# Kernel optimization log

Measured on AMD Instinct MI355X. Metric: run time of the kernel, lower is better.

## Reference

```python
import jax, jax.numpy as jnp
import numpy as np

B, T, C = 2, 2048, 1024
H = 16
D = C // H  # head_dim = 64
SCALE = D ** -0.5


def setup_inputs() -> dict:
    key = jax.random.key(0)
    ks = jax.random.split(key, 5)
    x = jax.random.normal(ks[0], (B, T, C), dtype=jnp.float32)
    # causal mask: -inf above diagonal, 0 elsewhere (module checks mask == -inf)
    neg_inf = jnp.float32(-jnp.inf)
    causal = jnp.where(jnp.tril(jnp.ones((T, T), dtype=bool)), 0.0, neg_inf)
    mask = causal[None, None, :, :].astype(jnp.float32)  # [1,1,T,T]
    # xavier_normal for [C, C] linear weights: std = sqrt(2/(C+C))
    std = float(np.sqrt(2.0 / (C + C)))
    wq = jax.random.normal(ks[1], (C, C), dtype=jnp.float32) * std
    wk = jax.random.normal(ks[2], (C, C), dtype=jnp.float32) * std
    wv = jax.random.normal(ks[3], (C, C), dtype=jnp.float32) * std
    wo = jax.random.normal(ks[4], (C, C), dtype=jnp.float32) * std
    return {"x": x, "mask": mask, "wq": wq, "wk": wk, "wv": wv, "wo": wo}


def reference(x, mask, wq, wk, wv, wo):
    # torch nn.Linear: y = x @ W.T
    q = jnp.einsum('btc,oc->bto', x, wq).reshape(B, T, H, D).transpose(0, 2, 1, 3)
    k = jnp.einsum('btc,oc->bto', x, wk).reshape(B, T, H, D).transpose(0, 2, 1, 3)
    v = jnp.einsum('btc,oc->bto', x, wv).reshape(B, T, H, D).transpose(0, 2, 1, 3)
    scores = jnp.einsum('bhqd,bhkd->bhqk', q, k) * SCALE  # [B,H,T,T]
    scores = jnp.where(mask == -jnp.inf, -jnp.inf, scores)
    attn = jax.nn.softmax(scores, axis=-1)
    out = jnp.einsum('bhqk,bhkd->bhqd', attn, v)  # [B,H,T,D]
    out = out.transpose(0, 2, 1, 3).reshape(B, T, C)
    return jnp.einsum('btc,oc->bto', out, wo)
```

## Files before the change

### kernel.cpp

```cpp
#include <hip/hip_runtime.h>
#include <hip/hip_bf16.h>


typedef __bf16 bf16_t;
typedef __bf16 bf16x8 __attribute__((ext_vector_type(8)));
typedef __bf16 bf16x4 __attribute__((ext_vector_type(4)));
typedef __bf16 bf16x2 __attribute__((ext_vector_type(2)));
typedef float  f32x4  __attribute__((ext_vector_type(4)));
typedef unsigned u32x4 __attribute__((ext_vector_type(4)));

__device__ __forceinline__ void gload_lds16(const bf16_t* g, bf16_t* l) {
  __builtin_amdgcn_global_load_lds((__attribute__((address_space(1))) void*)g,
                                   (__attribute__((address_space(3))) void*)l, 16, 0, 0);
}

__device__ __forceinline__ unsigned pack_bf16(float a, float b) {
  bf16x2 v; v[0] = (bf16_t)a; v[1] = (bf16_t)b;
  return __builtin_bit_cast(unsigned, v);
}

__device__ __forceinline__ float fexp2(float x) { return __builtin_amdgcn_exp2f(x); }

__global__ __launch_bounds__(256) void cvt_all(
    const float* __restrict__ x,  const float* __restrict__ i0, const float* __restrict__ i1,
    const float* __restrict__ i2, const float* __restrict__ i3,
    bf16_t* __restrict__ ox, bf16_t* __restrict__ o0, bf16_t* __restrict__ o1,
    bf16_t* __restrict__ o2, bf16_t* __restrict__ o3) {
  int blk = blockIdx.x;
  const float* in; bf16_t* out; int i;
  if (blk < 4096) { in = x; out = ox; i = blk * 256 + threadIdx.x; }
  else {
    int wb = blk - 4096;
    int which = wb >> 10;
    in  = (which == 0) ? i0 : (which == 1) ? i1 : (which == 2) ? i2 : i3;
    out = (which == 0) ? o0 : (which == 1) ? o1 : (which == 2) ? o2 : o3;
    i = (wb & 1023) * 256 + threadIdx.x;
  }
  float4 v = reinterpret_cast<const float4*>(in)[i];
  bf16x4 o;
  o[0] = (bf16_t)v.x; o[1] = (bf16_t)v.y; o[2] = (bf16_t)v.z; o[3] = (bf16_t)v.w;
  reinterpret_cast<bf16x4*>(out)[i] = o;
}

__global__ __launch_bounds__(256) void gemm_bt(
    const bf16_t* __restrict__ A,
    const bf16_t* __restrict__ W0, const bf16_t* __restrict__ W1, const bf16_t* __restrict__ W2,
    bf16_t* __restrict__ O0, bf16_t* __restrict__ O1, bf16_t* __restrict__ O2)
{
  __shared__ alignas(16) bf16_t As[64 * 64];
  __shared__ alignas(16) bf16_t Bs[128 * 64];
  const int K = 1024;
  const int t = threadIdx.x;
  const int lane = t & 63;
  const int w = t >> 6;
  const int wr = w >> 1, wc = w & 1;
  const int lo = lane & 15, hi = lane >> 4;
  const int m0 = blockIdx.x * 64, n0 = blockIdx.y * 128;

  const int mode = blockIdx.z;
  const bf16_t* Bw = (mode == 0) ? W0 : (mode == 1) ? W1 : W2;
  bf16_t* outb     = (mode == 0) ? O0 : (mode == 1) ? O1 : O2;

  f32x4 acc[2][4] = {};
  const int srow = t >> 3;
  const int sch  = t & 7;

  for (int k0 = 0; k0 < K; k0 += 64) {
#pragma unroll
    for (int r = 0; r < 2; ++r) {
      int row = r * 32 + srow;
      gload_lds16(A + (size_t)(m0 + row) * K + k0 + sch * 8, &As[row * 64 + sch * 8]);
    }
#pragma unroll
    for (int r = 0; r < 4; ++r) {
      int row = r * 32 + srow;
      gload_lds16(Bw + (size_t)(n0 + row) * K + k0 + sch * 8, &Bs[row * 64 + sch * 8]);
    }
    __syncthreads();
#pragma unroll
    for (int ks = 0; ks < 2; ++ks) {
      bf16x8 af[2], bfr[4];
#pragma unroll
      for (int i = 0; i < 2; ++i)
        af[i] = *reinterpret_cast<const bf16x8*>(&As[(wr * 32 + i * 16 + lo) * 64 + ks * 32 + hi * 8]);
#pragma unroll
      for (int j = 0; j < 4; ++j)
        bfr[j] = *reinterpret_cast<const bf16x8*>(&Bs[(wc * 64 + j * 16 + lo) * 64 + ks * 32 + hi * 8]);
#pragma unroll
      for (int i = 0; i < 2; ++i)
#pragma unroll
        for (int j = 0; j < 4; ++j)
          acc[i][j] = __builtin_amdgcn_mfma_f32_16x16x32_bf16(af[i], bfr[j], acc[i][j], 0, 0, 0);
    }
    __syncthreads();
  }

  if (mode == 2) {
#pragma unroll
    for (int i = 0; i < 2; ++i)
#pragma unroll
      for (int j = 0; j < 4; ++j) {
        int m = m0 + wr * 32 + i * 16 + hi * 4;
        int n = n0 + wc * 64 + j * 16 + lo;
        int b = m >> 11, tq = m & 2047;
        int h = (n >> 6) & 15, d = n & 63;
        bf16x4 pk;
#pragma unroll
        for (int r = 0; r < 4; ++r) pk[r] = (bf16_t)acc[i][j][r];
        *reinterpret_cast<bf16x4*>(
            &outb[((size_t)(b * 16 + h) * 64 + d) * 2048 + tq]) = pk;
      }
  } else {
#pragma unroll
    for (int i = 0; i < 2; ++i)
#pragma unroll
      for (int j = 0; j < 4; ++j)
#pragma unroll
        for (int r = 0; r < 4; ++r) {
          int m = m0 + wr * 32 + i * 16 + hi * 4 + r;
          int n = n0 + wc * 64 + j * 16 + lo;
          float v = acc[i][j][r];
          int b = m >> 11, tq = m & 2047;
          int h = n >> 6,  d  = n & 63;
          if (mode == 0) v *= 0.18033688011f;
          outb[((size_t)(b * 16 + h) * 2048 + tq) * 64 + d] = (bf16_t)v;
        }
  }
}

__global__ __launch_bounds__(256) void gemm_out(
    const bf16_t* __restrict__ A, const bf16_t* __restrict__ Wt, float* __restrict__ OF)
{
  __shared__ alignas(16) bf16_t As[64 * 64];
  __shared__ alignas(16) bf16_t Bs[128 * 64];
  const int K = 1024;
  const int t = threadIdx.x;
  const int lane = t & 63;
  const int w = t >> 6;
  const int wr = w >> 1, wc = w & 1;
  const int lo = lane & 15, hi = lane >> 4;
  const int m0 = blockIdx.x * 64, n0 = blockIdx.y * 128;

  f32x4 acc[2][4] = {};
  const int srow = t >> 3;
  const int sch  = t & 7;

  for (int k0 = 0; k0 < K; k0 += 64) {
#pragma unroll
    for (int r = 0; r < 2; ++r) {
      int row = r * 32 + srow;
      gload_lds16(A + (size_t)(m0 + row) * K + k0 + sch * 8, &As[row * 64 + sch * 8]);
    }
#pragma unroll
    for (int r = 0; r < 4; ++r) {
      int row = r * 32 + srow;
      gload_lds16(Wt + (size_t)(n0 + row) * K + k0 + sch * 8, &Bs[row * 64 + sch * 8]);
    }
    __syncthreads();
#pragma unroll
    for (int ks = 0; ks < 2; ++ks) {
      bf16x8 af[2], bfr[4];
#pragma unroll
      for (int i = 0; i < 2; ++i)
        af[i] = *reinterpret_cast<const bf16x8*>(&As[(wr * 32 + i * 16 + lo) * 64 + ks * 32 + hi * 8]);
#pragma unroll
      for (int j = 0; j < 4; ++j)
        bfr[j] = *reinterpret_cast<const bf16x8*>(&Bs[(wc * 64 + j * 16 + lo) * 64 + ks * 32 + hi * 8]);
#pragma unroll
      for (int i = 0; i < 2; ++i)
#pragma unroll
        for (int j = 0; j < 4; ++j)
          acc[i][j] = __builtin_amdgcn_mfma_f32_16x16x32_bf16(af[i], bfr[j], acc[i][j], 0, 0, 0);
    }
    __syncthreads();
  }

#pragma unroll
  for (int i = 0; i < 2; ++i)
#pragma unroll
    for (int j = 0; j < 4; ++j)
#pragma unroll
      for (int r = 0; r < 4; ++r) {
        int m = m0 + wr * 32 + i * 16 + hi * 4 + r;
        int n = n0 + wc * 64 + j * 16 + lo;
        OF[(size_t)m * 1024 + n] = acc[i][j][r];
      }
}

#define SLAB 8832

__global__ __launch_bounds__(256) void attn_fwd(
    const bf16_t* __restrict__ Q,
    const bf16_t* __restrict__ Km,
    const bf16_t* __restrict__ Vt,
    bf16_t* __restrict__ att)
{
  __shared__ alignas(16) char smem[4 * SLAB];
  const int t = threadIdx.x, lane = t & 63, w = t >> 6;
  const int lo = lane & 15, h = lane >> 4;
  const int blk = blockIdx.x;
  const int item = (blk & 7) * 128 + (blk >> 3);
  const int bh = item >> 5;
  const int pr = item & 31;
  const bf16_t* Qb = Q  + (size_t)bh * 2048 * 64;
  const bf16_t* Kb = Km + (size_t)bh * 2048 * 64;
  const bf16_t* Vb = Vt + (size_t)bh * 64 * 2048;
  float* accW = (float*)(smem + w * SLAB);
  float* lW   = (float*)(smem + w * SLAB + 8704);
  const int b = bh >> 4, hd = bh & 15;
  const int prow = 8 * (lo >> 2) + (lo & 3);

  auto run_tile = [&](int q0) {
    bf16x8 qf[2][2];
#pragma unroll
    for (int qt = 0; qt < 2; ++qt)
#pragma unroll
      for (int ks = 0; ks < 2; ++ks)
        qf[qt][ks] = *reinterpret_cast<const bf16x8*>(
            &Qb[(size_t)(q0 + qt * 16 + lo) * 64 + ks * 32 + h * 8]);

    f32x4 acc[2][4] = {};
    float lp[2] = {};
    const int kend = q0 + 32;
    for (int kb = w * 64; kb < kend; kb += 256) {
      bf16x8 kf[2][4];
#pragma unroll
      for (int ks = 0; ks < 2; ++ks)
#pragma unroll
        for (int kt = 0; kt < 4; ++kt) {
          int krow = kb + 32 * (kt & 1) + 4 * (kt >> 1) + prow;
          kf[ks][kt] = *reinterpret_cast<const bf16x8*>(
              &Kb[(size_t)krow * 64 + ks * 32 + h * 8]);
        }
      bf16x8 vf[2][4];
#pragma unroll
      for (int kh = 0; kh < 2; ++kh)
#pragma unroll
        for (int dt = 0; dt < 4; ++dt)
          vf[kh][dt] = *reinterpret_cast<const bf16x8*>(
              &Vb[(size_t)(dt * 16 + lo) * 2048 + kb + kh * 32 + h * 8]);
      f32x4 s_t[4][2] = {};
#pragma unroll
      for (int ks = 0; ks < 2; ++ks)
#pragma unroll
        for (int kt = 0; kt < 4; ++kt)
#pragma unroll
          for (int qt = 0; qt < 2; ++qt)
            s_t[kt][qt] = __builtin_amdgcn_mfma_f32_16x16x32_bf16(kf[ks][kt], qf[qt][ks], s_t[kt][qt], 0, 0, 0);
      if (kb + 63 >= q0) {
#pragma unroll
        for (int kt = 0; kt < 4; ++kt)
#pragma unroll
          for (int qt = 0; qt < 2; ++qt)
#pragma unroll
            for (int r = 0; r < 4; ++r) {
              int kg = kb + 32 * (kt & 1) + 8 * h + 4 * (kt >> 1) + r;
              int qg = q0 + qt * 16 + lo;
              if (kg > qg) s_t[kt][qt][r] = -__builtin_inff();
            }
      }
#pragma unroll
      for (int kt = 0; kt < 4; ++kt)
#pragma unroll
        for (int qt = 0; qt < 2; ++qt)
#pragma unroll
          for (int r = 0; r < 4; ++r) {
            float p = fexp2(s_t[kt][qt][r]);
            s_t[kt][qt][r] = p;
            lp[qt] += p;
          }
#pragma unroll
      for (int ks2 = 0; ks2 < 2; ++ks2)
#pragma unroll
        for (int qt = 0; qt < 2; ++qt) {
          u32x4 au;
          au[0] = pack_bf16(s_t[ks2][qt][0], s_t[ks2][qt][1]);
          au[1] = pack_bf16(s_t[ks2][qt][2], s_t[ks2][qt][3]);
          au[2] = pack_bf16(s_t[ks2 + 2][qt][0], s_t[ks2 + 2][qt][1]);
          au[3] = pack_bf16(s_t[ks2 + 2][qt][2], s_t[ks2 + 2][qt][3]);
          bf16x8 pa = __builtin_bit_cast(bf16x8, au);
#pragma unroll
          for (int dt = 0; dt < 4; ++dt)
            acc[qt][dt] = __builtin_amdgcn_mfma_f32_16x16x32_bf16(pa, vf[ks2][dt], acc[qt][dt], 0, 0, 0);
        }
    }

    float lrow[2];
#pragma unroll
    for (int qt = 0; qt < 2; ++qt) {
      float v = lp[qt];
      v += __shfl_xor(v, 16);
      v += __shfl_xor(v, 32);
      lrow[qt] = v;
    }

#pragma unroll
    for (int qt = 0; qt < 2; ++qt) {
#pragma unroll
      for (int r = 0; r < 4; ++r) {
        int row = qt * 16 + h * 4 + r;
#pragma unroll
        for (int dt = 0; dt < 4; ++dt)
          accW[row * 68 + dt * 16 + lo] = acc[qt][dt][r];
      }
      if (h == 0) lW[qt * 16 + lo] = lrow[qt];
    }
    __syncthreads();

    {
      const int row = t >> 3, c0 = (t & 7) * 8;
      float lsum = 0.f, o[8] = {};
#pragma unroll
      for (int w2 = 0; w2 < 4; ++w2) {
        lsum += ((const float*)(smem + w2 * SLAB + 8704))[row];
        const float* a2 = (const float*)(smem + w2 * SLAB) + row * 68 + c0;
#pragma unroll
        for (int j = 0; j < 8; ++j) o[j] += a2[j];
      }
      float inv = 1.f / lsum;
      bf16x8 ov;
#pragma unroll
      for (int j = 0; j < 8; ++j) ov[j] = (bf16_t)(o[j] * inv);
      *reinterpret_cast<bf16x8*>(&att[((size_t)(b * 2048 + q0 + row)) * 1024 + hd * 64 + c0]) = ov;
    }
    __syncthreads();
  };

  run_tile((63 - pr) * 32);
  run_tile(pr * 32);
}

extern "C" void kernel_launch(void* const* d_in, const int* in_sizes, int n_in,
                              void* d_out, int out_size, void* d_ws, size_t ws_size,
                              hipStream_t stream) {
  (void)in_sizes; (void)n_in; (void)out_size; (void)ws_size;
  const float* x  = (const float*)d_in[0];
  const float* wq = (const float*)d_in[2];
  const float* wk = (const float*)d_in[3];
  const float* wv = (const float*)d_in[4];
  const float* wo = (const float*)d_in[5];
  float* out = (float*)d_out;

  char* ws = (char*)d_ws;
  const size_t SZ_X = (size_t)4096 * 1024 * 2;
  const size_t SZ_W = (size_t)1024 * 1024 * 2;
  bf16_t* xb  = (bf16_t*)(ws);
  bf16_t* wqb = (bf16_t*)(ws + SZ_X);
  bf16_t* wkb = (bf16_t*)(ws + SZ_X + 1 * SZ_W);
  bf16_t* wvb = (bf16_t*)(ws + SZ_X + 2 * SZ_W);
  bf16_t* wob = (bf16_t*)(ws + SZ_X + 3 * SZ_W);
  bf16_t* qw  = (bf16_t*)(ws + 1 * SZ_X + 4 * SZ_W);
  bf16_t* kw  = (bf16_t*)(ws + 2 * SZ_X + 4 * SZ_W);
  bf16_t* vtw = (bf16_t*)(ws + 3 * SZ_X + 4 * SZ_W);
  bf16_t* att = xb;

  cvt_all<<<8192, 256, 0, stream>>>(x, wq, wk, wv, wo, xb, wqb, wkb, wvb, wob);

  gemm_bt<<<dim3(64, 8, 3), 256, 0, stream>>>(xb, wqb, wkb, wvb, qw, kw, vtw);
  attn_fwd<<<1024, 256, 0, stream>>>(qw, kw, vtw, att);
  gemm_out<<<dim3(64, 8), 256, 0, stream>>>(att, wob, out);
}
```

Measured before the change: 146.0 us.

## Stage partial attention outputs in bf16 LDS and load K/V per sub-step

The per-wave partial output accumulators are now staged in shared memory as bf16 instead of fp32, roughly halving the LDS slab per wave, and the cross-wave reduction reads them with 16-byte vector loads. K and V fragments are loaded per k-slice just before use rather than all up front, which lowers live vector registers. Together these aim to cut LDS footprint and register pressure to raise occupancy. The cost is an extra bf16 rounding of the unnormalized partial sums before the reduction, and less load latency hiding because the loads are issued later.

```diff
diff --git a/kernel.cpp b/kernel.cpp
--- a/kernel.cpp
+++ b/kernel.cpp
@@ -187,7 +187,7 @@
       }
 }
 
-#define SLAB 8832
+#define SLAB 4736
 
 __global__ __launch_bounds__(256) void attn_fwd(
     const bf16_t* __restrict__ Q,
@@ -205,8 +205,8 @@
   const bf16_t* Qb = Q  + (size_t)bh * 2048 * 64;
   const bf16_t* Kb = Km + (size_t)bh * 2048 * 64;
   const bf16_t* Vb = Vt + (size_t)bh * 64 * 2048;
-  float* accW = (float*)(smem + w * SLAB);
-  float* lW   = (float*)(smem + w * SLAB + 8704);
+  bf16_t* accW = (bf16_t*)(smem + w * SLAB);
+  float*  lW   = (float*)(smem + w * SLAB + 4608);
   const int b = bh >> 4, hd = bh & 15;
   const int prow = 8 * (lo >> 2) + (lo & 3);
 
@@ -223,30 +223,22 @@
     float lp[2] = {};
     const int kend = q0 + 32;
     for (int kb = w * 64; kb < kend; kb += 256) {
-      bf16x8 kf[2][4];
-#pragma unroll
-      for (int ks = 0; ks < 2; ++ks)
+      f32x4 s_t[4][2] = {};
+#pragma unroll
+      for (int ks = 0; ks < 2; ++ks) {
+        bf16x8 kf[4];
 #pragma unroll
         for (int kt = 0; kt < 4; ++kt) {
           int krow = kb + 32 * (kt & 1) + 4 * (kt >> 1) + prow;
-          kf[ks][kt] = *reinterpret_cast<const bf16x8*>(
+          kf[kt] = *reinterpret_cast<const bf16x8*>(
               &Kb[(size_t)krow * 64 + ks * 32 + h * 8]);
         }
-      bf16x8 vf[2][4];
-#pragma unroll
-      for (int kh = 0; kh < 2; ++kh)
-#pragma unroll
-        for (int dt = 0; dt < 4; ++dt)
-          vf[kh][dt] = *reinterpret_cast<const bf16x8*>(
-              &Vb[(size_t)(dt * 16 + lo) * 2048 + kb + kh * 32 + h * 8]);
-      f32x4 s_t[4][2] = {};
-#pragma unroll
-      for (int ks = 0; ks < 2; ++ks)
 #pragma unroll
         for (int kt = 0; kt < 4; ++kt)
 #pragma unroll
           for (int qt = 0; qt < 2; ++qt)
-            s_t[kt][qt] = __builtin_amdgcn_mfma_f32_16x16x32_bf16(kf[ks][kt], qf[qt][ks], s_t[kt][qt], 0, 0, 0);
+            s_t[kt][qt] = __builtin_amdgcn_mfma_f32_16x16x32_bf16(kf[kt], qf[qt][ks], s_t[kt][qt], 0, 0, 0);
+      }
       if (kb + 63 >= q0) {
 #pragma unroll
         for (int kt = 0; kt < 4; ++kt)
@@ -270,7 +262,12 @@
             lp[qt] += p;
           }
 #pragma unroll
-      for (int ks2 = 0; ks2 < 2; ++ks2)
+      for (int ks2 = 0; ks2 < 2; ++ks2) {
+        bf16x8 vf[4];
+#pragma unroll
+        for (int dt = 0; dt < 4; ++dt)
+          vf[dt] = *reinterpret_cast<const bf16x8*>(
+              &Vb[(size_t)(dt * 16 + lo) * 2048 + kb + ks2 * 32 + h * 8]);
 #pragma unroll
         for (int qt = 0; qt < 2; ++qt) {
           u32x4 au;
@@ -281,8 +278,9 @@
           bf16x8 pa = __builtin_bit_cast(bf16x8, au);
 #pragma unroll
           for (int dt = 0; dt < 4; ++dt)
-            acc[qt][dt] = __builtin_amdgcn_mfma_f32_16x16x32_bf16(pa, vf[ks2][dt], acc[qt][dt], 0, 0, 0);
+            acc[qt][dt] = __builtin_amdgcn_mfma_f32_16x16x32_bf16(pa, vf[dt], acc[qt][dt], 0, 0, 0);
         }
+      }
     }
 
     float lrow[2];
@@ -301,7 +299,7 @@
         int row = qt * 16 + h * 4 + r;
 #pragma unroll
         for (int dt = 0; dt < 4; ++dt)
-          accW[row * 68 + dt * 16 + lo] = acc[qt][dt][r];
+          accW[row * 72 + dt * 16 + lo] = (bf16_t)acc[qt][dt][r];
       }
       if (h == 0) lW[qt * 16 + lo] = lrow[qt];
     }
@@ -312,10 +310,11 @@
       float lsum = 0.f, o[8] = {};
 #pragma unroll
       for (int w2 = 0; w2 < 4; ++w2) {
-        lsum += ((const float*)(smem + w2 * SLAB + 8704))[row];
-        const float* a2 = (const float*)(smem + w2 * SLAB) + row * 68 + c0;
-#pragma unroll
-        for (int j = 0; j < 8; ++j) o[j] += a2[j];
+        lsum += ((const float*)(smem + w2 * SLAB + 4608))[row];
+        bf16x8 a2 = *reinterpret_cast<const bf16x8*>(
+            (const bf16_t*)(smem + w2 * SLAB) + row * 72 + c0);
+#pragma unroll
+        for (int j = 0; j < 8; ++j) o[j] += (float)a2[j];
       }
       float inv = 1.f / lsum;
       bf16x8 ov;
```

Measured after the change: 145.7 us. No clear change (-0.2%).
